# Performance work log

Measured on AMD Instinct MI355X. Metric: run time of the kernel, lower is better.

Reference implementation:

```python
import jax, jax.numpy as jnp
import numpy as np

TAU_U = 1.0
TAU_L = 0.05
EPS = 1e-12  # torch F.normalize eps


def setup_inputs() -> dict:
    key = jax.random.key(0)
    ks = jax.random.split(key, 8)
    N, D, B = 100000, 128, 8192
    x1 = jax.random.normal(ks[0], (N, D), dtype=jnp.float32)
    x2 = jax.random.normal(ks[1], (N, D), dtype=jnp.float32)
    x1_index = jax.random.randint(ks[2], (B,), 0, N, dtype=jnp.int64 if jax.config.jax_enable_x64 else jnp.int32)
    x2_index = jax.random.randint(ks[3], (B,), 0, N, dtype=jnp.int64 if jax.config.jax_enable_x64 else jnp.int32)
    # Linear params (torch Linear default init: U(-1/sqrt(fan_in), 1/sqrt(fan_in)))
    lim1 = 1.0 / np.sqrt(D)
    W1 = jax.random.uniform(ks[4], (D, D), minval=-lim1, maxval=lim1, dtype=jnp.float32)
    b1 = jax.random.uniform(ks[5], (D,), minval=-lim1, maxval=lim1, dtype=jnp.float32)
    W2 = jax.random.uniform(ks[6], (1, D), minval=-lim1, maxval=lim1, dtype=jnp.float32)
    b2 = jax.random.uniform(ks[7], (1,), minval=-lim1, maxval=lim1, dtype=jnp.float32)
    return {"x1": x1, "x2": x2, "x1_index": x1_index, "x2_index": x2_index,
            "W1": W1, "b1": b1, "W2": W2, "b2": b2}


def _l2norm(x):
    # matches torch F.normalize(dim=1) for 2-D input
    n = jnp.sqrt(jnp.sum(x * x, axis=-1, keepdims=True))
    return x / jnp.maximum(n, EPS)


def reference(x1, x2, x1_index, x2_index, W1, b1, W2, b2):
    x1_feat = _l2norm(x1[x1_index])          # [B, D]
    x2_feat = _l2norm(x2[x2_index])          # [B, D]

    h = x1_feat * x2_feat                    # [B, D]
    h = h @ W1.T + b1                        # lin1
    h = jnp.where(h >= 0, h, 0.2 * h)        # leaky_relu(0.2)
    s = jax.nn.sigmoid(h @ W2.T + b2)        # [B, 1]
    ssl_temp = (TAU_U - TAU_L) * (1.0 - s) + TAU_L   # [B, 1]

    pos = jnp.sum(x1_feat * x2_feat, axis=-1)         # [B]
    # NOTE: [B] / [B,1] broadcasts to [B,B] exactly like torch
    pos_rating = jnp.exp(pos / ssl_temp)              # [B, B]

    tot = x1_feat @ x2_feat.T                          # [B, B]
    tot_rating = jnp.sum(jnp.exp(tot / ssl_temp), axis=1)  # [B]

    ssl_temp_avg = jnp.mean(ssl_temp)
    return (pos_rating, tot_rating, ssl_temp_avg)
```

## Files before the change

kernel.cpp:

```cpp
#include <hip/hip_runtime.h>
#include <stdint.h>

typedef __bf16 bf16x8 __attribute__((ext_vector_type(8)));
typedef float f32x4 __attribute__((ext_vector_type(4)));
typedef __attribute__((address_space(3))) uint32_t as3u32;
typedef const __attribute__((address_space(1))) uint32_t as1u32;

#define B_TOT 8192
#define DD 128
#define OUT_TOT 67108864UL
#define OUT_AVG 67117056UL

__device__ inline unsigned short f2bf(float x){
  union { float f; uint32_t u; } v; v.f = x;
  return (unsigned short)((v.u + 0x7fffu + ((v.u >> 16) & 1u)) >> 16);
}

__global__ __launch_bounds__(256) void k_feat(const float* __restrict__ x1,
    const float* __restrict__ x2, const int* __restrict__ i1a, const int* __restrict__ i2a,
    unsigned short* __restrict__ f1b, unsigned short* __restrict__ f2b,
    unsigned short* __restrict__ hb, float* __restrict__ posw, float* __restrict__ out){
  int tid = threadIdx.x;
  int gid = blockIdx.x * 256 + tid;
  if (gid <= 8192) out[OUT_TOT + gid] = 0.f;
  int w = tid >> 6, l = tid & 63;
  int b = blockIdx.x * 4 + w;
  const float2* r1 = (const float2*)(x1 + (size_t)i1a[b] * DD);
  const float2* r2 = (const float2*)(x2 + (size_t)i2a[b] * DD);
  float2 v1 = r1[l], v2 = r2[l];
  float s1 = v1.x * v1.x + v1.y * v1.y;
  float s2 = v2.x * v2.x + v2.y * v2.y;
  #pragma unroll
  for (int o = 32; o; o >>= 1){ s1 += __shfl_xor(s1, o); s2 += __shfl_xor(s2, o); }
  float inv1 = 1.f / fmaxf(sqrtf(s1), 1e-12f);
  float inv2 = 1.f / fmaxf(sqrtf(s2), 1e-12f);
  float f1x = v1.x * inv1, f1y = v1.y * inv1;
  float f2x = v2.x * inv2, f2y = v2.y * inv2;
  float hx = f1x * f2x, hy = f1y * f2y;
  float ps = hx + hy;
  #pragma unroll
  for (int o = 32; o; o >>= 1) ps += __shfl_xor(ps, o);
  unsigned int u1 = (unsigned int)f2bf(f1x) | ((unsigned int)f2bf(f1y) << 16);
  unsigned int u2 = (unsigned int)f2bf(f2x) | ((unsigned int)f2bf(f2y) << 16);
  unsigned int uh = (unsigned int)f2bf(hx)  | ((unsigned int)f2bf(hy)  << 16);
  ((unsigned int*)f1b)[b * 64 + l] = u1;
  ((unsigned int*)f2b)[b * 64 + l] = u2;
  ((unsigned int*)hb)[b * 64 + l]  = uh;
  if (l == 0) posw[b] = ps;
}

__device__ inline void stage_tile(const unsigned short* g, unsigned short* s){
  int tid = threadIdx.x;
  #pragma unroll
  for (int it = 0; it < 8; ++it){
    int c = tid + it * 256;
    int row = c >> 4, cc = c & 15;
    int src = (row << 4) + (cc ^ (row & 7));
    __builtin_amdgcn_global_load_lds((as1u32*)(g + src * 8),
                                     (as3u32*)(s + c * 8), 16, 0, 0);
  }
}

__device__ inline void mfma_tile(const unsigned short* As, const unsigned short* Bs,
                                 f32x4 acc[4][4]){
  int tid = threadIdx.x;
  int w = tid >> 6, l = tid & 63;
  int wr = (w >> 1) * 64, wc = (w & 1) * 64;
  int lo = l & 15, hi = l >> 4;
  f32x4 zero = {0.f, 0.f, 0.f, 0.f};
  #pragma unroll
  for (int m = 0; m < 4; ++m)
    #pragma unroll
    for (int n = 0; n < 4; ++n) acc[m][n] = zero;
  #pragma unroll
  for (int kk = 0; kk < 4; ++kk){
    bf16x8 af[4], bfv[4];
    #pragma unroll
    for (int m = 0; m < 4; ++m){
      int row = wr + m * 16 + lo;
      af[m] = *(const bf16x8*)(As + row * 128 + ((kk * 4 + hi) ^ (row & 7)) * 8);
    }
    #pragma unroll
    for (int n = 0; n < 4; ++n){
      int row = wc + n * 16 + lo;
      bfv[n] = *(const bf16x8*)(Bs + row * 128 + ((kk * 4 + hi) ^ (row & 7)) * 8);
    }
    #pragma unroll
    for (int m = 0; m < 4; ++m)
      #pragma unroll
      for (int n = 0; n < 4; ++n)
        acc[m][n] = __builtin_amdgcn_mfma_f32_16x16x32_bf16(af[m], bfv[n], acc[m][n], 0, 0, 0);
  }
}

__global__ __launch_bounds__(256) void k_lin(const unsigned short* __restrict__ hb,
    const float* __restrict__ W1, const float* __restrict__ b1,
    const float* __restrict__ W2, const float* __restrict__ b2,
    float* __restrict__ rTw, float* __restrict__ out){
  __shared__ __align__(16) unsigned short As[16384];
  __shared__ __align__(16) unsigned short Bs[16384];
  __shared__ float zpart[2][128];
  __shared__ float s4[4];
  int i0 = blockIdx.x * 128;
  int tid = threadIdx.x;
  stage_tile(hb + (size_t)i0 * 128, As);
  #pragma unroll
  for (int it = 0; it < 8; ++it){
    int c = tid + it * 256;
    int row = c >> 4, cc = c & 15;
    int src = (row << 4) + (cc ^ (row & 7));
    const float4* g4 = (const float4*)(W1 + src * 8);
    float4 a = g4[0], b = g4[1];
    unsigned short t8[8];
    t8[0] = f2bf(a.x); t8[1] = f2bf(a.y); t8[2] = f2bf(a.z); t8[3] = f2bf(a.w);
    t8[4] = f2bf(b.x); t8[5] = f2bf(b.y); t8[6] = f2bf(b.z); t8[7] = f2bf(b.w);
    *(uint4*)(Bs + c * 8) = *(uint4*)t8;
  }
  asm volatile("s_waitcnt vmcnt(0)" ::: "memory");
  __syncthreads();
  f32x4 acc[4][4];
  mfma_tile(As, Bs, acc);
  int w = tid >> 6, l = tid & 63;
  int wrb = (w >> 1) * 64, wcb = (w & 1) * 64, lo = l & 15, hi = l >> 4;
  float w2v[4], b1v[4];
  #pragma unroll
  for (int n = 0; n < 4; ++n){ int col = wcb + n * 16 + lo; w2v[n] = W2[col]; b1v[n] = b1[col]; }
  #pragma unroll
  for (int m = 0; m < 4; ++m){
    #pragma unroll
    for (int q = 0; q < 4; ++q){
      float p = 0.f;
      #pragma unroll
      for (int n = 0; n < 4; ++n){
        float hv = acc[m][n][q] + b1v[n];
        hv = hv >= 0.f ? hv : 0.2f * hv;
        p += hv * w2v[n];
      }
      p += __shfl_xor(p, 1); p += __shfl_xor(p, 2);
      p += __shfl_xor(p, 4); p += __shfl_xor(p, 8);
      if (lo == 0) zpart[w & 1][wrb + m * 16 + hi * 4 + q] = p;
    }
  }
  __syncthreads();
  float Tloc = 0.f;
  if (tid < 128){
    float z = zpart[0][tid] + zpart[1][tid] + b2[0];
    float s = 1.f / (1.f + __expf(-z));
    float T = 0.95f * (1.f - s) + 0.05f;
    rTw[i0 + tid] = 1.f / T;
    Tloc = T;
  }
  float v = Tloc;
  #pragma unroll
  for (int o = 32; o; o >>= 1) v += __shfl_xor(v, o);
  if ((tid & 63) == 0) s4[tid >> 6] = v;
  __syncthreads();
  if (tid == 0) atomicAdd(out + OUT_AVG, (s4[0] + s4[1] + s4[2] + s4[3]) * (1.0f / 8192.0f));
}

__global__ __launch_bounds__(256, 2) void k_tot(const unsigned short* __restrict__ f1b,
    const unsigned short* __restrict__ f2b, const float* __restrict__ rTw,
    const float* __restrict__ posw, float* __restrict__ out){
  __shared__ __align__(16) unsigned short Buf[16384];
  __shared__ __align__(16) float posS[8192];
  __shared__ __align__(16) float rS[128];
  __shared__ __align__(16) float rQ[16];
  int s = (blockIdx.x & 7) * 64 + (blockIdx.x >> 3);
  int rt = s & 63, ctg = s >> 6;
  int tid = threadIdx.x, w = tid >> 6, l = tid & 63;
  int wr = (w >> 1) * 64, wc = (w & 1) * 64;
  int lo = l & 15, hi = l >> 4;
  stage_tile(f1b + (size_t)rt * 16384, Buf);
  #pragma unroll
  for (int it = 0; it < 8; ++it){
    int c = tid + it * 256;
    __builtin_amdgcn_global_load_lds((as1u32*)(posw + c * 4),
                                     (as3u32*)(posS + c * 4), 16, 0, 0);
  }
  if (tid < 32)
    __builtin_amdgcn_global_load_lds((as1u32*)(rTw + rt * 128 + tid * 4),
                                     (as3u32*)(rS + tid * 4), 16, 0, 0);
  if (tid < 4)
    __builtin_amdgcn_global_load_lds((as1u32*)(rTw + s * 16 + tid * 4),
                                     (as3u32*)(rQ + tid * 4), 16, 0, 0);
  asm volatile("s_waitcnt vmcnt(0)" ::: "memory");
  __builtin_amdgcn_s_barrier();
  bf16x8 af[4][4];
  #pragma unroll
  for (int kk = 0; kk < 4; ++kk)
    #pragma unroll
    for (int m = 0; m < 4; ++m){
      int row = wr + m * 16 + lo;
      af[kk][m] = *(const bf16x8*)(Buf + row * 128 + ((kk * 4 + hi) ^ (row & 7)) * 8);
    }
  asm volatile("s_waitcnt lgkmcnt(0)" ::: "memory");
  __builtin_amdgcn_s_barrier();
  stage_tile(f2b + (size_t)(ctg * 8) * 16384, Buf);
  asm volatile("s_waitcnt vmcnt(0)" ::: "memory");
  __builtin_amdgcn_s_barrier();
  float pacc[4][4] = {{0.f,0.f,0.f,0.f},{0.f,0.f,0.f,0.f},{0.f,0.f,0.f,0.f},{0.f,0.f,0.f,0.f}};
  int half = w & 1, rsel = w >> 1;
  #pragma unroll 1
  for (int c8 = 0; c8 < 8; ++c8){
    int ct = ctg * 8 + c8;
    f32x4 acc[4][4];
    f32x4 zero = {0.f,0.f,0.f,0.f};
    #pragma unroll
    for (int m = 0; m < 4; ++m)
      #pragma unroll
      for (int n = 0; n < 4; ++n) acc[m][n] = zero;
    #pragma unroll
    for (int kk = 0; kk < 4; ++kk){
      bf16x8 bfv[4];
      #pragma unroll
      for (int n = 0; n < 4; ++n){
        int row = wc + n * 16 + lo;
        bfv[n] = *(const bf16x8*)(Buf + row * 128 + ((kk * 4 + hi) ^ (row & 7)) * 8);
      }
      #pragma unroll
      for (int m = 0; m < 4; ++m)
        #pragma unroll
        for (int n = 0; n < 4; ++n)
          acc[m][n] = __builtin_amdgcn_mfma_f32_16x16x32_bf16(af[kk][m], bfv[n], acc[m][n], 0, 0, 0);
    }
    asm volatile("s_waitcnt lgkmcnt(0)" ::: "memory");
    __builtin_amdgcn_s_barrier();
    if (c8 < 7) stage_tile(f2b + (size_t)(ct + 1) * 16384, Buf);
    __builtin_amdgcn_sched_barrier(0);
    #pragma unroll
    for (int m = 0; m < 4; ++m)
      #pragma unroll
      for (int q = 0; q < 4; ++q){
        float r = rS[wr + m * 16 + hi * 4 + q];
        pacc[m][q] += __expf(acc[m][0][q] * r) + __expf(acc[m][1][q] * r)
                    + __expf(acc[m][2][q] * r) + __expf(acc[m][3][q] * r);
      }
    {
      int rowi = s * 16 + c8 * 2 + rsel;
      float rr = rQ[c8 * 2 + rsel];
      float* obase = out + (size_t)rowi * B_TOT + half * 4096;
      #pragma unroll
      for (int j = 0; j < 16; ++j){
        f32x4 p = *(const f32x4*)&posS[half * 4096 + j * 256 + l * 4];
        f32x4 e;
        e.x = __expf(p.x * rr); e.y = __expf(p.y * rr);
        e.z = __expf(p.z * rr); e.w = __expf(p.w * rr);
        __builtin_nontemporal_store(e, (f32x4*)(obase + j * 256 + l * 4));
      }
    }
    if (c8 < 7){
      asm volatile("s_waitcnt vmcnt(16)" ::: "memory");
      __builtin_amdgcn_s_barrier();
    }
  }
  #pragma unroll
  for (int m = 0; m < 4; ++m)
    #pragma unroll
    for (int q = 0; q < 4; ++q){
      float p = pacc[m][q];
      p += __shfl_xor(p, 1); p += __shfl_xor(p, 2);
      p += __shfl_xor(p, 4); p += __shfl_xor(p, 8);
      if (lo == 0) atomicAdd(out + OUT_TOT + rt * 128 + wr + m * 16 + hi * 4 + q, p);
    }
}

extern "C" void kernel_launch(void* const* d_in, const int* in_sizes, int n_in,
                              void* d_out, int out_size, void* d_ws, size_t ws_size,
                              hipStream_t stream){
  const float* x1 = (const float*)d_in[0];
  const float* x2 = (const float*)d_in[1];
  const int*   i1 = (const int*)d_in[2];
  const int*   i2 = (const int*)d_in[3];
  const float* W1 = (const float*)d_in[4];
  const float* b1 = (const float*)d_in[5];
  const float* W2 = (const float*)d_in[6];
  const float* b2 = (const float*)d_in[7];
  float* out = (float*)d_out;
  char* ws = (char*)d_ws;
  unsigned short* hb   = (unsigned short*)(ws);
  unsigned short* f1b  = (unsigned short*)(ws + 2097152);
  unsigned short* f2b  = (unsigned short*)(ws + 4194304);
  float* posw  = (float*)(ws + 6291456);
  float* rTw   = (float*)(ws + 6324224);

  hipLaunchKernelGGL(k_feat,  dim3(2048), dim3(256), 0, stream, x1, x2, i1, i2, f1b, f2b, hb, posw, out);
  hipLaunchKernelGGL(k_lin,   dim3(64),   dim3(256), 0, stream, hb, W1, b1, W2, b2, rTw, out);
  hipLaunchKernelGGL(k_tot,   dim3(512),  dim3(256), 0, stream, f1b, f2b, rTw, posw, out);
}
```

Baseline: 87.41 us.

## Split pos_rating outer-product write out of k_tot into separate streaming kernel

Moves the B×B exp(pos/T) output write out of the GEMM kernel k_tot, which had it interleaved with the MFMA loop, into a new standalone kernel k_pr. k_pr keeps the pos vector in registers and writes 4 rows per block. This drops 32 KB of LDS from k_tot and simplifies its loop. It trades overlap of the 256 MB store stream with the tensor-core work for an extra launch that runs serially after the GEMM, and it switches from nontemporal to plain stores.

```diff
diff --git a/kernel.cpp b/kernel.cpp
--- a/kernel.cpp
+++ b/kernel.cpp
@@ -160,29 +160,18 @@
 
 __global__ __launch_bounds__(256, 2) void k_tot(const unsigned short* __restrict__ f1b,
     const unsigned short* __restrict__ f2b, const float* __restrict__ rTw,
-    const float* __restrict__ posw, float* __restrict__ out){
+    float* __restrict__ out){
   __shared__ __align__(16) unsigned short Buf[16384];
-  __shared__ __align__(16) float posS[8192];
   __shared__ __align__(16) float rS[128];
-  __shared__ __align__(16) float rQ[16];
   int s = (blockIdx.x & 7) * 64 + (blockIdx.x >> 3);
   int rt = s & 63, ctg = s >> 6;
   int tid = threadIdx.x, w = tid >> 6, l = tid & 63;
   int wr = (w >> 1) * 64, wc = (w & 1) * 64;
   int lo = l & 15, hi = l >> 4;
   stage_tile(f1b + (size_t)rt * 16384, Buf);
-  #pragma unroll
-  for (int it = 0; it < 8; ++it){
-    int c = tid + it * 256;
-    __builtin_amdgcn_global_load_lds((as1u32*)(posw + c * 4),
-                                     (as3u32*)(posS + c * 4), 16, 0, 0);
-  }
   if (tid < 32)
     __builtin_amdgcn_global_load_lds((as1u32*)(rTw + rt * 128 + tid * 4),
                                      (as3u32*)(rS + tid * 4), 16, 0, 0);
-  if (tid < 4)
-    __builtin_amdgcn_global_load_lds((as1u32*)(rTw + s * 16 + tid * 4),
-                                     (as3u32*)(rQ + tid * 4), 16, 0, 0);
   asm volatile("s_waitcnt vmcnt(0)" ::: "memory");
   __builtin_amdgcn_s_barrier();
   bf16x8 af[4][4];
@@ -199,7 +188,6 @@
   asm volatile("s_waitcnt vmcnt(0)" ::: "memory");
   __builtin_amdgcn_s_barrier();
   float pacc[4][4] = {{0.f,0.f,0.f,0.f},{0.f,0.f,0.f,0.f},{0.f,0.f,0.f,0.f},{0.f,0.f,0.f,0.f}};
-  int half = w & 1, rsel = w >> 1;
   #pragma unroll 1
   for (int c8 = 0; c8 < 8; ++c8){
     int ct = ctg * 8 + c8;
@@ -226,7 +214,6 @@
     asm volatile("s_waitcnt lgkmcnt(0)" ::: "memory");
     __builtin_amdgcn_s_barrier();
     if (c8 < 7) stage_tile(f2b + (size_t)(ct + 1) * 16384, Buf);
-    __builtin_amdgcn_sched_barrier(0);
     #pragma unroll
     for (int m = 0; m < 4; ++m)
       #pragma unroll
@@ -235,21 +222,8 @@
         pacc[m][q] += __expf(acc[m][0][q] * r) + __expf(acc[m][1][q] * r)
                     + __expf(acc[m][2][q] * r) + __expf(acc[m][3][q] * r);
       }
-    {
-      int rowi = s * 16 + c8 * 2 + rsel;
-      float rr = rQ[c8 * 2 + rsel];
-      float* obase = out + (size_t)rowi * B_TOT + half * 4096;
-      #pragma unroll
-      for (int j = 0; j < 16; ++j){
-        f32x4 p = *(const f32x4*)&posS[half * 4096 + j * 256 + l * 4];
-        f32x4 e;
-        e.x = __expf(p.x * rr); e.y = __expf(p.y * rr);
-        e.z = __expf(p.z * rr); e.w = __expf(p.w * rr);
-        __builtin_nontemporal_store(e, (f32x4*)(obase + j * 256 + l * 4));
-      }
-    }
     if (c8 < 7){
-      asm volatile("s_waitcnt vmcnt(16)" ::: "memory");
+      asm volatile("s_waitcnt vmcnt(0)" ::: "memory");
       __builtin_amdgcn_s_barrier();
     }
   }
@@ -262,6 +236,28 @@
       p += __shfl_xor(p, 4); p += __shfl_xor(p, 8);
       if (lo == 0) atomicAdd(out + OUT_TOT + rt * 128 + wr + m * 16 + hi * 4 + q, p);
     }
+}
+
+__global__ __launch_bounds__(256) void k_pr(const float* __restrict__ posw,
+    const float* __restrict__ rTw, float* __restrict__ out){
+  int tid = threadIdx.x;
+  int r0 = blockIdx.x * 4;
+  f32x4 p[8];
+  #pragma unroll
+  for (int c = 0; c < 8; ++c) p[c] = *(const f32x4*)(posw + (c * 256 + tid) * 4);
+  float4 rr4 = *(const float4*)(rTw + r0);
+  float rr[4] = {rr4.x, rr4.y, rr4.z, rr4.w};
+  #pragma unroll
+  for (int r = 0; r < 4; ++r){
+    float* ob = out + (size_t)(r0 + r) * B_TOT;
+    #pragma unroll
+    for (int c = 0; c < 8; ++c){
+      f32x4 e;
+      e.x = __expf(p[c].x * rr[r]); e.y = __expf(p[c].y * rr[r]);
+      e.z = __expf(p[c].z * rr[r]); e.w = __expf(p[c].w * rr[r]);
+      *(f32x4*)(ob + (c * 256 + tid) * 4) = e;
+    }
+  }
 }
 
 extern "C" void kernel_launch(void* const* d_in, const int* in_sizes, int n_in,
@@ -285,5 +281,6 @@
 
   hipLaunchKernelGGL(k_feat,  dim3(2048), dim3(256), 0, stream, x1, x2, i1, i2, f1b, f2b, hb, posw, out);
   hipLaunchKernelGGL(k_lin,   dim3(64),   dim3(256), 0, stream, hb, W1, b1, W2, b2, rTw, out);
-  hipLaunchKernelGGL(k_tot,   dim3(512),  dim3(256), 0, stream, f1b, f2b, rTw, posw, out);
-}
+  hipLaunchKernelGGL(k_tot,   dim3(512),  dim3(256), 0, stream, f1b, f2b, rTw, out);
+  hipLaunchKernelGGL(k_pr,    dim3(2048), dim3(256), 0, stream, posw, rTw, out);
+}
```

After: 86.56 us. About the same (-1.0%).
